# Optimization experiments

Hardware: AMD Instinct MI355X
Metric: run time of the kernel (lower is better)

## Reference

```python
import jax, jax.numpy as jnp
import numpy as np

N_NODES = 50000
N_EDGES = 800000
D_IN = 512
D_OUT = 512


def setup_inputs() -> dict:
    key = jax.random.key(0)
    k1, k2, k3, k4, k5 = jax.random.split(key, 5)
    x = jax.random.normal(k1, (N_NODES, D_IN), dtype=jnp.float32)
    weight = jax.random.normal(k2, (D_IN, D_OUT), dtype=jnp.float32) * (1.0 / np.sqrt(D_IN))
    edge_weight = jax.random.uniform(k3, (N_EDGES,), dtype=jnp.float32)
    edge_src = jax.random.randint(k4, (N_EDGES,), 0, N_NODES, dtype=jnp.int32)
    edge_dst = jax.random.randint(k5, (N_EDGES,), 0, N_NODES, dtype=jnp.int32)
    return {"x": x, "weight": weight, "edge_weight": edge_weight,
            "edge_src": edge_src, "edge_dst": edge_dst}


def reference(x, weight, edge_weight, edge_src, edge_dst):
    # support = x @ W  (dense GEMM, [N, D_out])
    support = jnp.matmul(x, weight)
    # output = adj @ support  (SpMM in COO form):
    # gather source rows, scale by edge weight, scatter-add into destinations
    msgs = support[edge_src] * edge_weight[:, None]          # [E, D_out]
    output = jax.ops.segment_sum(msgs, edge_dst, num_segments=N_NODES)
    return output
```

## Files before the change

### kernel.cpp

```cpp
#include <hip/hip_runtime.h>
#include <stdint.h>

#define N_NODES 50000
#define N_EDGES 800000
#define D 512
#define M_PAD 50048
#define CAP 64
#define CAPSH 6

#define FILL_NB 3125
#define WT_NB   1024
#define CVT_NB  25024

typedef __attribute__((ext_vector_type(8))) __bf16 bf16x8;
typedef __attribute__((ext_vector_type(4))) float f32x4;

static __device__ __forceinline__ unsigned short f2bf(float f) {
  unsigned u = __float_as_uint(f);
  u += 0x7fff + ((u >> 16) & 1);
  return (unsigned short)(u >> 16);
}
static __device__ __forceinline__ float bf2f(unsigned short h) {
  return __uint_as_float(((unsigned)h) << 16);
}

static __device__ __forceinline__ void gload_lds16(const void* g, void* l) {
  __builtin_amdgcn_global_load_lds((const __attribute__((address_space(1))) unsigned*)g,
                                   (__attribute__((address_space(3))) unsigned*)l, 16, 0, 0);
}

__global__ __launch_bounds__(256) void k_mega(const float* __restrict__ x,
                                              const float* __restrict__ w,
                                              const float* __restrict__ ew,
                                              const int* __restrict__ esrc,
                                              const int* __restrict__ edst,
                                              unsigned short* __restrict__ xb,
                                              unsigned short* __restrict__ wt,
                                              int* __restrict__ cur,
                                              int2* __restrict__ cew) {
  int bid = blockIdx.x;
  if (bid < FILL_NB) {
    int e = bid * 256 + threadIdx.x;
    int d = edst[e];
    int r = atomicAdd(&cur[d], 1);
    if (r < CAP) cew[(d << CAPSH) + r] = make_int2(esrc[e], __float_as_int(ew[e]));
    return;
  }
  bid -= FILL_NB;
  if (bid < WT_NB) {
    int n = bid >> 1;
    int k = ((bid & 1) << 8) + threadIdx.x;
    wt[n * D + k] = f2bf(w[k * D + n]);
    return;
  }
  bid -= WT_NB;
  long long base = ((long long)bid * 256 + threadIdx.x) * 4;
  int row = (int)(base >> 9);
  ushort4 o;
  if (row < N_NODES) {
    float4 v = *(const float4*)(x + base);
    o.x = f2bf(v.x); o.y = f2bf(v.y); o.z = f2bf(v.z); o.w = f2bf(v.w);
  } else {
    o.x = 0; o.y = 0; o.z = 0; o.w = 0;
  }
  *(ushort4*)(xb + base) = o;
}

__global__ __launch_bounds__(256) void k_gemm(const unsigned short* __restrict__ A,
                                              const unsigned short* __restrict__ Bt,
                                              unsigned short* __restrict__ C) {
  __shared__ unsigned short lds_a[128 * 32];
  __shared__ unsigned short lds_b[128 * 32];
  const int tid  = threadIdx.x;
  const int bm   = blockIdx.x >> 2;
  const int bn   = blockIdx.x & 3;
  const int m0   = bm * 128, n0 = bn * 128;
  const int wave = tid >> 6, lane = tid & 63;
  const int wm   = wave & 1, wn = wave >> 1;
  const int l15  = lane & 15, quad = lane >> 4;

  f32x4 acc[4][4];
#pragma unroll
  for (int i = 0; i < 4; i++)
#pragma unroll
    for (int j = 0; j < 4; j++) acc[i][j] = f32x4{0.f, 0.f, 0.f, 0.f};

  for (int kt = 0; kt < D / 32; ++kt) {
    const int k0 = kt * 32;
    __syncthreads();
#pragma unroll
    for (int c = 0; c < 2; c++) {
      int i = c * 256 + wave * 64 + lane;
      int r = i >> 2, kc = (i & 3) << 3;
      gload_lds16(&A[(long long)(m0 + r) * D + k0 + kc], &lds_a[(c * 256 + wave * 64) * 8]);
      gload_lds16(&Bt[(long long)(n0 + r) * D + k0 + kc], &lds_b[(c * 256 + wave * 64) * 8]);
    }
    __syncthreads();
    bf16x8 af[4], bfr[4];
#pragma unroll
    for (int t = 0; t < 4; t++) {
      af[t]  = *(const bf16x8*)&lds_a[(wm * 64 + t * 16 + l15) * 32 + quad * 8];
      bfr[t] = *(const bf16x8*)&lds_b[(wn * 64 + t * 16 + l15) * 32 + quad * 8];
    }
#pragma unroll
    for (int i = 0; i < 4; i++)
#pragma unroll
      for (int j = 0; j < 4; j++)
        acc[i][j] = __builtin_amdgcn_mfma_f32_16x16x32_bf16(af[i], bfr[j], acc[i][j], 0, 0, 0);
  }
#pragma unroll
  for (int i = 0; i < 4; i++)
#pragma unroll
    for (int j = 0; j < 4; j++)
#pragma unroll
      for (int r = 0; r < 4; r++) {
        int row = m0 + wm * 64 + i * 16 + quad * 4 + r;
        int col = n0 + wn * 64 + j * 16 + l15;
        C[(long long)row * D + col] = f2bf(acc[i][j][r]);
      }
}

__global__ __launch_bounds__(256) void k_agg(const int* __restrict__ cur,
                                             const int2* __restrict__ cew,
                                             const unsigned short* __restrict__ S,
                                             float* __restrict__ out) {
  __shared__ float s_part[4 * 512];
  const int node  = blockIdx.x;
  int cnt = cur[node];
  cnt = (cnt > CAP) ? CAP : cnt;
  const int start = node << CAPSH, end = start + cnt;
  const int wave  = threadIdx.x >> 6, lane = threadIdx.x & 63;
  float a[8];
#pragma unroll
  for (int k = 0; k < 8; k++) a[k] = 0.f;

#define EDGE_FMA(V, W)                                             \
  do {                                                             \
    a[0] = fmaf(W, bf2f((unsigned short)(V.x & 0xffffu)), a[0]);   \
    a[1] = fmaf(W, bf2f((unsigned short)(V.x >> 16)),     a[1]);   \
    a[2] = fmaf(W, bf2f((unsigned short)(V.y & 0xffffu)), a[2]);   \
    a[3] = fmaf(W, bf2f((unsigned short)(V.y >> 16)),     a[3]);   \
    a[4] = fmaf(W, bf2f((unsigned short)(V.z & 0xffffu)), a[4]);   \
    a[5] = fmaf(W, bf2f((unsigned short)(V.z >> 16)),     a[5]);   \
    a[6] = fmaf(W, bf2f((unsigned short)(V.w & 0xffffu)), a[6]);   \
    a[7] = fmaf(W, bf2f((unsigned short)(V.w >> 16)),     a[7]);   \
  } while (0)

#define GATHER(P) (*(const uint4*)(S + (size_t)(P).x * D + lane * 8))

  int e = start + wave;
  for (; e + 4 < end; e += 8) {
    int2 p0 = cew[e], p1 = cew[e + 4];
    uint4 v0 = GATHER(p0);
    uint4 v1 = GATHER(p1);
    EDGE_FMA(v0, __int_as_float(p0.y));
    EDGE_FMA(v1, __int_as_float(p1.y));
  }
  if (e < end) {
    int2 p0 = cew[e];
    uint4 v0 = GATHER(p0);
    EDGE_FMA(v0, __int_as_float(p0.y));
  }
#undef GATHER
#undef EDGE_FMA

  float4* sp = (float4*)&s_part[wave * 512 + lane * 8];
  sp[0] = make_float4(a[0], a[1], a[2], a[3]);
  sp[1] = make_float4(a[4], a[5], a[6], a[7]);
  __syncthreads();
  int col = threadIdx.x * 2;
  float2 r0 = *(const float2*)&s_part[0 * 512 + col];
  float2 r1 = *(const float2*)&s_part[1 * 512 + col];
  float2 r2 = *(const float2*)&s_part[2 * 512 + col];
  float2 r3 = *(const float2*)&s_part[3 * 512 + col];
  float2 res = make_float2(r0.x + r1.x + r2.x + r3.x, r0.y + r1.y + r2.y + r3.y);
  typedef __attribute__((ext_vector_type(2))) float f32x2;
  f32x2 rv = {res.x, res.y};
  __builtin_nontemporal_store(rv, (f32x2*)(out + (size_t)node * D + col));
}

extern "C" void kernel_launch(void* const* d_in, const int* in_sizes, int n_in,
                              void* d_out, int out_size, void* d_ws, size_t ws_size,
                              hipStream_t stream) {
  const float* x    = (const float*)d_in[0];
  const float* w    = (const float*)d_in[1];
  const float* ew   = (const float*)d_in[2];
  const int*   esrc = (const int*)d_in[3];
  const int*   edst = (const int*)d_in[4];
  float* out = (float*)d_out;

  char* p = (char*)d_ws;
  auto align256 = [](size_t v) { return (v + 255) & ~(size_t)255; };
  unsigned short* xb = (unsigned short*)p;  p += align256((size_t)M_PAD * D * 2);
  unsigned short* sb = (unsigned short*)p;  p += align256((size_t)M_PAD * D * 2);
  unsigned short* wt = (unsigned short*)p;  p += align256((size_t)D * D * 2);
  int*   cur  = (int*)p;   p += align256((size_t)N_NODES * 4);
  int2*  cew  = (int2*)p;  p += align256((size_t)N_NODES * CAP * 8);

  hipMemsetAsync(cur, 0, (size_t)N_NODES * 4, stream);
  k_mega<<<FILL_NB + WT_NB + CVT_NB, 256, 0, stream>>>(x, w, ew, esrc, edst, xb, wt, cur, cew);
  k_gemm<<<391 * 4, 256, 0, stream>>>(xb, wt, sb);
  k_agg<<<N_NODES, 256, 0, stream>>>(cur, cew, sb, out);
}
```

Baseline: 378.1 us.

## Move edge bucketing into GEMM kernel and remap GEMM tiles per XCD

The atomic edge-bucketing work moves out of the conversion kernel and into the GEMM launch as extra leading blocks, so the latency-bound scatter can overlap with MFMA tiles. GEMM block IDs are also remapped so that consecutive tiles land on the same XCD, which is meant to improve L2 reuse of the A rows shared across the four N tiles. The fill blocks declare the GEMM's LDS even though they do not use it, which may limit how many fill blocks are resident at once.

```diff
diff --git a/kernel.cpp b/kernel.cpp
--- a/kernel.cpp
+++ b/kernel.cpp
@@ -11,6 +11,7 @@
 #define FILL_NB 3125
 #define WT_NB   1024
 #define CVT_NB  25024
+#define GEMM_NB 1564
 
 typedef __attribute__((ext_vector_type(8))) __bf16 bf16x8;
 typedef __attribute__((ext_vector_type(4))) float f32x4;
@@ -29,24 +30,11 @@
                                    (__attribute__((address_space(3))) unsigned*)l, 16, 0, 0);
 }
 
-__global__ __launch_bounds__(256) void k_mega(const float* __restrict__ x,
-                                              const float* __restrict__ w,
-                                              const float* __restrict__ ew,
-                                              const int* __restrict__ esrc,
-                                              const int* __restrict__ edst,
-                                              unsigned short* __restrict__ xb,
-                                              unsigned short* __restrict__ wt,
-                                              int* __restrict__ cur,
-                                              int2* __restrict__ cew) {
+__global__ __launch_bounds__(256) void k_pre(const float* __restrict__ x,
+                                             const float* __restrict__ w,
+                                             unsigned short* __restrict__ xb,
+                                             unsigned short* __restrict__ wt) {
   int bid = blockIdx.x;
-  if (bid < FILL_NB) {
-    int e = bid * 256 + threadIdx.x;
-    int d = edst[e];
-    int r = atomicAdd(&cur[d], 1);
-    if (r < CAP) cew[(d << CAPSH) + r] = make_int2(esrc[e], __float_as_int(ew[e]));
-    return;
-  }
-  bid -= FILL_NB;
   if (bid < WT_NB) {
     int n = bid >> 1;
     int k = ((bid & 1) << 8) + threadIdx.x;
@@ -66,14 +54,32 @@
   *(ushort4*)(xb + base) = o;
 }
 
-__global__ __launch_bounds__(256) void k_gemm(const unsigned short* __restrict__ A,
-                                              const unsigned short* __restrict__ Bt,
-                                              unsigned short* __restrict__ C) {
+__global__ __launch_bounds__(256) void k_gf(const unsigned short* __restrict__ A,
+                                            const unsigned short* __restrict__ Bt,
+                                            unsigned short* __restrict__ C,
+                                            const int* __restrict__ esrc,
+                                            const int* __restrict__ edst,
+                                            const float* __restrict__ ew,
+                                            int* __restrict__ cur,
+                                            int2* __restrict__ cew) {
   __shared__ unsigned short lds_a[128 * 32];
   __shared__ unsigned short lds_b[128 * 32];
+
+  if (blockIdx.x < FILL_NB) {
+    int e = blockIdx.x * 256 + threadIdx.x;
+    int d = edst[e];
+    int r = atomicAdd(&cur[d], 1);
+    if (r < CAP) cew[(d << CAPSH) + r] = make_int2(esrc[e], __float_as_int(ew[e]));
+    return;
+  }
+
+  const int orig = blockIdx.x - FILL_NB;
+  const int q = GEMM_NB / 8, r = GEMM_NB % 8;
+  const int xcd = orig & 7, j = orig >> 3;
+  const int wgid = (xcd < r ? xcd * (q + 1) : r * (q + 1) + (xcd - r) * q) + j;
+  const int bm = wgid >> 2, bn = wgid & 3;
+
   const int tid  = threadIdx.x;
-  const int bm   = blockIdx.x >> 2;
-  const int bn   = blockIdx.x & 3;
   const int m0   = bm * 128, n0 = bn * 128;
   const int wave = tid >> 6, lane = tid & 63;
   const int wm   = wave & 1, wn = wave >> 1;
@@ -83,7 +89,7 @@
 #pragma unroll
   for (int i = 0; i < 4; i++)
 #pragma unroll
-    for (int j = 0; j < 4; j++) acc[i][j] = f32x4{0.f, 0.f, 0.f, 0.f};
+    for (int jj = 0; jj < 4; jj++) acc[i][jj] = f32x4{0.f, 0.f, 0.f, 0.f};
 
   for (int kt = 0; kt < D / 32; ++kt) {
     const int k0 = kt * 32;
@@ -91,9 +97,9 @@
 #pragma unroll
     for (int c = 0; c < 2; c++) {
       int i = c * 256 + wave * 64 + lane;
-      int r = i >> 2, kc = (i & 3) << 3;
-      gload_lds16(&A[(long long)(m0 + r) * D + k0 + kc], &lds_a[(c * 256 + wave * 64) * 8]);
-      gload_lds16(&Bt[(long long)(n0 + r) * D + k0 + kc], &lds_b[(c * 256 + wave * 64) * 8]);
+      int rr = i >> 2, kc = (i & 3) << 3;
+      gload_lds16(&A[(long long)(m0 + rr) * D + k0 + kc], &lds_a[(c * 256 + wave * 64) * 8]);
+      gload_lds16(&Bt[(long long)(n0 + rr) * D + k0 + kc], &lds_b[(c * 256 + wave * 64) * 8]);
     }
     __syncthreads();
     bf16x8 af[4], bfr[4];
@@ -105,18 +111,19 @@
 #pragma unroll
     for (int i = 0; i < 4; i++)
 #pragma unroll
-      for (int j = 0; j < 4; j++)
-        acc[i][j] = __builtin_amdgcn_mfma_f32_16x16x32_bf16(af[i], bfr[j], acc[i][j], 0, 0, 0);
-  }
+      for (int jj = 0; jj < 4; jj++)
+        acc[i][jj] = __builtin_amdgcn_mfma_f32_16x16x32_bf16(af[i], bfr[jj], acc[i][jj], 0, 0, 0);
+  }
+
 #pragma unroll
   for (int i = 0; i < 4; i++)
 #pragma unroll
-    for (int j = 0; j < 4; j++)
-#pragma unroll
-      for (int r = 0; r < 4; r++) {
-        int row = m0 + wm * 64 + i * 16 + quad * 4 + r;
-        int col = n0 + wn * 64 + j * 16 + l15;
-        C[(long long)row * D + col] = f2bf(acc[i][j][r]);
+    for (int jj = 0; jj < 4; jj++)
+#pragma unroll
+      for (int rr = 0; rr < 4; rr++) {
+        int row = m0 + wm * 64 + i * 16 + quad * 4 + rr;
+        int col = n0 + wn * 64 + jj * 16 + l15;
+        C[(long long)row * D + col] = f2bf(acc[i][jj][rr]);
       }
 }
 
@@ -198,7 +205,7 @@
   int2*  cew  = (int2*)p;  p += align256((size_t)N_NODES * CAP * 8);
 
   hipMemsetAsync(cur, 0, (size_t)N_NODES * 4, stream);
-  k_mega<<<FILL_NB + WT_NB + CVT_NB, 256, 0, stream>>>(x, w, ew, esrc, edst, xb, wt, cur, cew);
-  k_gemm<<<391 * 4, 256, 0, stream>>>(xb, wt, sb);
+  k_pre<<<WT_NB + CVT_NB, 256, 0, stream>>>(x, w, xb, wt);
+  k_gf<<<FILL_NB + GEMM_NB, 256, 0, stream>>>(xb, wt, sb, esrc, edst, ew, cur, cew);
   k_agg<<<N_NODES, 256, 0, stream>>>(cur, cew, sb, out);
 }
```

After: 386.7 us. 1.02x slower.

## Retile GEMM to 64-row blocks spanning full 512-column output width

Applied to the files above, without the earlier changes.

The GEMM now uses 64x512 tiles instead of 128x128, so each block loads its A rows once and every wave computes a 64x128 slab with 32 accumulators. This removes the fourfold re-reading of A across column blocks but reloads the whole B slice per K step into a larger LDS buffer. Register pressure roughly doubles, and the launch bound is set to allow 2 blocks per CU.

```diff
diff --git a/kernel.cpp b/kernel.cpp
--- a/kernel.cpp
+++ b/kernel.cpp
@@ -11,6 +11,7 @@
 #define FILL_NB 3125
 #define WT_NB   1024
 #define CVT_NB  25024
+#define GEMM_NB 782
 
 typedef __attribute__((ext_vector_type(8))) __bf16 bf16x8;
 typedef __attribute__((ext_vector_type(4))) float f32x4;
@@ -66,56 +67,58 @@
   *(ushort4*)(xb + base) = o;
 }
 
-__global__ __launch_bounds__(256) void k_gemm(const unsigned short* __restrict__ A,
-                                              const unsigned short* __restrict__ Bt,
-                                              unsigned short* __restrict__ C) {
-  __shared__ unsigned short lds_a[128 * 32];
-  __shared__ unsigned short lds_b[128 * 32];
+__global__ __launch_bounds__(256, 2) void k_gemm(const unsigned short* __restrict__ A,
+                                                 const unsigned short* __restrict__ Bt,
+                                                 unsigned short* __restrict__ C) {
+  __shared__ unsigned short lds_a[64 * 32];
+  __shared__ unsigned short lds_b[512 * 32];
   const int tid  = threadIdx.x;
-  const int bm   = blockIdx.x >> 2;
-  const int bn   = blockIdx.x & 3;
-  const int m0   = bm * 128, n0 = bn * 128;
+  const int m0   = blockIdx.x * 64;
   const int wave = tid >> 6, lane = tid & 63;
-  const int wm   = wave & 1, wn = wave >> 1;
   const int l15  = lane & 15, quad = lane >> 4;
-
-  f32x4 acc[4][4];
+  const int ncol0 = wave * 128;
+
+  f32x4 acc[4][8];
 #pragma unroll
   for (int i = 0; i < 4; i++)
 #pragma unroll
-    for (int j = 0; j < 4; j++) acc[i][j] = f32x4{0.f, 0.f, 0.f, 0.f};
+    for (int j = 0; j < 8; j++) acc[i][j] = f32x4{0.f, 0.f, 0.f, 0.f};
+
+  const int ra = tid >> 2, kca = (tid & 3) << 3;
 
   for (int kt = 0; kt < D / 32; ++kt) {
     const int k0 = kt * 32;
     __syncthreads();
-#pragma unroll
-    for (int c = 0; c < 2; c++) {
+    gload_lds16(&A[(long long)(m0 + ra) * D + k0 + kca], &lds_a[(wave * 64) * 8]);
+#pragma unroll
+    for (int c = 0; c < 8; c++) {
       int i = c * 256 + wave * 64 + lane;
-      int r = i >> 2, kc = (i & 3) << 3;
-      gload_lds16(&A[(long long)(m0 + r) * D + k0 + kc], &lds_a[(c * 256 + wave * 64) * 8]);
-      gload_lds16(&Bt[(long long)(n0 + r) * D + k0 + kc], &lds_b[(c * 256 + wave * 64) * 8]);
+      int rb = i >> 2, kcb = (i & 3) << 3;
+      gload_lds16(&Bt[(long long)rb * D + k0 + kcb], &lds_b[(c * 256 + wave * 64) * 8]);
     }
     __syncthreads();
-    bf16x8 af[4], bfr[4];
-#pragma unroll
-    for (int t = 0; t < 4; t++) {
-      af[t]  = *(const bf16x8*)&lds_a[(wm * 64 + t * 16 + l15) * 32 + quad * 8];
-      bfr[t] = *(const bf16x8*)&lds_b[(wn * 64 + t * 16 + l15) * 32 + quad * 8];
-    }
+    bf16x8 af[4], bfr[8];
+#pragma unroll
+    for (int t = 0; t < 4; t++)
+      af[t] = *(const bf16x8*)&lds_a[(t * 16 + l15) * 32 + quad * 8];
+#pragma unroll
+    for (int t = 0; t < 8; t++)
+      bfr[t] = *(const bf16x8*)&lds_b[(ncol0 + t * 16 + l15) * 32 + quad * 8];
 #pragma unroll
     for (int i = 0; i < 4; i++)
 #pragma unroll
-      for (int j = 0; j < 4; j++)
+      for (int j = 0; j < 8; j++)
         acc[i][j] = __builtin_amdgcn_mfma_f32_16x16x32_bf16(af[i], bfr[j], acc[i][j], 0, 0, 0);
   }
+
 #pragma unroll
   for (int i = 0; i < 4; i++)
 #pragma unroll
-    for (int j = 0; j < 4; j++)
+    for (int j = 0; j < 8; j++)
 #pragma unroll
       for (int r = 0; r < 4; r++) {
-        int row = m0 + wm * 64 + i * 16 + quad * 4 + r;
-        int col = n0 + wn * 64 + j * 16 + l15;
+        int row = m0 + i * 16 + quad * 4 + r;
+        int col = ncol0 + j * 16 + l15;
         C[(long long)row * D + col] = f2bf(acc[i][j][r]);
       }
 }
@@ -199,6 +202,6 @@
 
   hipMemsetAsync(cur, 0, (size_t)N_NODES * 4, stream);
   k_mega<<<FILL_NB + WT_NB + CVT_NB, 256, 0, stream>>>(x, w, ew, esrc, edst, xb, wt, cur, cew);
-  k_gemm<<<391 * 4, 256, 0, stream>>>(xb, wt, sb);
+  k_gemm<<<GEMM_NB, 256, 0, stream>>>(xb, wt, sb);
   k_agg<<<N_NODES, 256, 0, stream>>>(cur, cew, sb, out);
 }
```

After: 382.3 us. No clear change (+1.1%).
